# Kernel optimization log

Hardware: AMD Instinct MI355X
Metric: run time of the kernel (lower is better)

The kernel has to match this reference:

```python
import jax, jax.numpy as jnp
import numpy as np

EPS = 1.1920929e-07  # torch.finfo(float32).eps, used by F.rms_norm default

def rope(x, cos, sin):
    # x: [B,T,H,D]; cos/sin: [1,T,1,D//2]
    d = x.shape[-1] // 2
    x1, x2 = x[..., :d], x[..., d:]
    return jnp.concatenate([x1 * cos + x2 * sin, -x1 * sin + x2 * cos], axis=-1)

def rmsnorm(x):
    return x * jax.lax.rsqrt(jnp.mean(x * x, axis=-1, keepdims=True) + EPS)

def setup_inputs() -> dict:
    key = jax.random.key(0)
    ks = jax.random.split(key, 9)
    B, T, E = 2, 2048, 1024
    Hkv, D = 4, 64
    return {
        "x": jax.random.normal(ks[0], (B, T, E), jnp.float32),
        "ve": jax.random.normal(ks[1], (B, T, Hkv * D), jnp.float32),
        "cos": jax.random.normal(ks[2], (1, T, 1, D // 2), jnp.float32),
        "sin": jax.random.normal(ks[3], (1, T, 1, D // 2), jnp.float32),
        "Wq": jax.random.normal(ks[4], (E, E), jnp.float32) * 0.02,
        "Wk": jax.random.normal(ks[5], (Hkv * D, E), jnp.float32) * 0.02,
        "Wv": jax.random.normal(ks[6], (Hkv * D, E), jnp.float32) * 0.02,
        "Wproj": jax.random.normal(ks[7], (E, E), jnp.float32) * 0.02,
        "Wgate": jax.random.normal(ks[8], (Hkv, 32), jnp.float32) * 0.02,
        "window_size": 1024,
    }

def reference(x, ve, cos, sin, Wq, Wk, Wv, Wproj, Wgate, window_size):
    B, T, E = x.shape
    H, Hkv, D = 16, 4, 64
    G = H // Hkv  # GQA group size
    q = (x @ Wq.T).reshape(B, T, H, D)
    k = (x @ Wk.T).reshape(B, T, Hkv, D)
    v = (x @ Wv.T).reshape(B, T, Hkv, D)
    # value-embedding gating
    gate = 2.0 * jax.nn.sigmoid(x[..., :32] @ Wgate.T)          # [B,T,Hkv]
    v = v + gate[..., None] * ve.reshape(B, T, Hkv, D)
    # RoPE then QK RMS-norm
    q = rmsnorm(rope(q, cos, sin))
    k = rmsnorm(rope(k, cos, sin))
    # to [B,H,T,D]; repeat-interleave kv heads for GQA (matches torch enable_gqa)
    q = q.transpose(0, 2, 1, 3)
    k = jnp.repeat(k.transpose(0, 2, 1, 3), G, axis=1)
    v = jnp.repeat(v.transpose(0, 2, 1, 3), G, axis=1)
    # causal + sliding-window boolean mask
    row = jnp.arange(T)[:, None]
    col = jnp.arange(T)[None, :]
    mask = (col <= row) & (col >= row - window_size)            # [T,T]
    scale = 1.0 / jnp.sqrt(jnp.float32(D))
    scores = jnp.einsum("bhqd,bhkd->bhqk", q, k) * scale
    scores = jnp.where(mask, scores, -jnp.inf)
    p = jax.nn.softmax(scores, axis=-1)
    y = jnp.einsum("bhqk,bhkd->bhqd", p, v)
    y = y.transpose(0, 2, 1, 3).reshape(B, T, E)
    return y @ Wproj.T
```

## Files before the change

### kernel.cpp

```cpp
#include <hip/hip_runtime.h>


typedef float f32x4 __attribute__((ext_vector_type(4)));
typedef short s16x8 __attribute__((ext_vector_type(8)));
typedef short s16x4 __attribute__((ext_vector_type(4)));
typedef _Float16 f16x4 __attribute__((ext_vector_type(4)));

__device__ __forceinline__ unsigned short f2bf(float f) {
  unsigned u = __float_as_uint(f);
  u += 0x7fffu + ((u >> 16) & 1u);
  return (unsigned short)(u >> 16);
}
__device__ __forceinline__ unsigned short h16(float f) {
  _Float16 h = (_Float16)f;
  return __builtin_bit_cast(unsigned short, h);
}

__device__ __forceinline__ float fexp2(float x) {
#if __has_builtin(__builtin_amdgcn_exp2f)
  return __builtin_amdgcn_exp2f(x);
#else
  return __expf(x * 0.69314718f);
#endif
}

__device__ __forceinline__ void gl2lds16(const unsigned short* g, unsigned short* l) {
  __builtin_amdgcn_global_load_lds((const __attribute__((address_space(1))) unsigned int*)g,
                                   (__attribute__((address_space(3))) unsigned int*)l, 16, 0, 0);
}

__global__ __launch_bounds__(256) void cvt_gate(
    const float* __restrict__ x, const float* __restrict__ wq, const float* __restrict__ wk,
    const float* __restrict__ wv, const float* __restrict__ wp, const float* __restrict__ wgate,
    unsigned short* __restrict__ xb, unsigned short* __restrict__ wqkv,
    unsigned short* __restrict__ wpj, float* __restrict__ gatep) {
  int blk = blockIdx.x;
  if (blk < 6656) {
    int i = blk * 256 + threadIdx.x;
    const float* s;
    unsigned short* d;
    if (i < 1048576) { s = x; d = xb; }
    else if (i < 1310720) { i -= 1048576; s = wq; d = wqkv; }
    else if (i < 1376256) { i -= 1310720; s = wk; d = wqkv + 1048576; }
    else if (i < 1441792) { i -= 1376256; s = wv; d = wqkv + 1310720; }
    else { i -= 1441792; s = wp; d = wpj; }
    float4 v = ((const float4*)s)[i];
    ushort4 o;
    o.x = f2bf(v.x); o.y = f2bf(v.y); o.z = f2bf(v.z); o.w = f2bf(v.w);
    ((ushort4*)d)[i] = o;
  } else {
    int i = (blk - 6656) * 256 + threadIdx.x;
    int bt = i >> 2, h = i & 3;
    const float4* xp = (const float4*)(x + (size_t)bt * 1024);
    const float4* wpt = (const float4*)(wgate + h * 32);
    float s = 0.f;
#pragma unroll
    for (int j = 0; j < 8; ++j) {
      float4 a = xp[j], b = wpt[j];
      s += a.x * b.x + a.y * b.y + a.z * b.z + a.w * b.w;
    }
    gatep[i] = 2.f / (1.f + __expf(-s));
  }
}

__global__ __launch_bounds__(256) void gemm_qkv(
    const unsigned short* __restrict__ A, const unsigned short* __restrict__ B,
    const float* __restrict__ cosp, const float* __restrict__ sinp,
    const float* __restrict__ gatep, const float* __restrict__ ve,
    unsigned short* __restrict__ q_r, unsigned short* __restrict__ k_r,
    unsigned short* __restrict__ vp2) {
  __shared__ unsigned short smem[24576];
  unsigned short* As = smem;
  unsigned short* Bs = smem + 8192;
  const int K = 1024;
  int bn = blockIdx.x, bm = blockIdx.y;
  int t = threadIdx.x;
  int w = t >> 6, lane = t & 63;
  int c = lane & 15, g = lane >> 4;
  int wm = w >> 1, wn = w & 1;

  f32x4 acc[2][4];
#pragma unroll
  for (int i = 0; i < 2; ++i)
#pragma unroll
    for (int j = 0; j < 4; ++j) acc[i][j] = (f32x4){0.f, 0.f, 0.f, 0.f};

  const unsigned short* Ab = A + (size_t)(bm * 64) * K;
  const unsigned short* Bb = B + (size_t)(bn * 128) * K;
  int srow = lane >> 4;
  int sgrp = lane & 15;

  for (int k0 = 0; k0 < K; k0 += 128) {
#pragma unroll
    for (int j = 0; j < 4; ++j) {
      int r0 = w * 16 + j * 4;
      int r = r0 + srow;
      gl2lds16(Ab + (size_t)r * K + k0 + (sgrp ^ (r & 7)) * 8, As + r0 * 128);
    }
#pragma unroll
    for (int j = 0; j < 8; ++j) {
      int r0 = w * 32 + j * 4;
      int r = r0 + srow;
      gl2lds16(Bb + (size_t)r * K + k0 + (sgrp ^ (r & 7)) * 8, Bs + r0 * 128);
    }
    __syncthreads();
#pragma unroll
    for (int kk = 0; kk < 4; ++kk) {
      int sw = ((kk * 4 + g) ^ (c & 7)) * 8;
      s16x8 af[2], bf[4];
#pragma unroll
      for (int mt = 0; mt < 2; ++mt)
        af[mt] = *(const s16x8*)(As + (wm * 32 + mt * 16 + c) * 128 + sw);
#pragma unroll
      for (int nt = 0; nt < 4; ++nt)
        bf[nt] = *(const s16x8*)(Bs + (wn * 64 + nt * 16 + c) * 128 + sw);
#pragma unroll
      for (int mt = 0; mt < 2; ++mt)
#pragma unroll
        for (int nt = 0; nt < 4; ++nt)
          acc[mt][nt] = __builtin_amdgcn_mfma_f32_16x16x32_bf16(af[mt], bf[nt], acc[mt][nt], 0, 0, 0);
    }
    __syncthreads();
  }

  const float QSCL = 0.125f * 1.44269504f;
  if (bn < 10) {
    unsigned short* eb = smem + w * 2176;
#pragma unroll
    for (int mt = 0; mt < 2; ++mt) {
#pragma unroll
      for (int r = 0; r < 4; ++r) {
        int lrow = mt * 16 + g * 4 + r;
        int rowg = bm * 64 + wm * 32 + lrow;
        int tt = rowg & 2047;
        float v0 = acc[mt][0][r], v1 = acc[mt][1][r], v2 = acc[mt][2][r], v3 = acc[mt][3][r];
        float cs0 = cosp[tt * 32 + c], sn0 = sinp[tt * 32 + c];
        float cs1 = cosp[tt * 32 + 16 + c], sn1 = sinp[tt * 32 + 16 + c];
        float r0 = v0 * cs0 + v2 * sn0;
        float r1 = v1 * cs1 + v3 * sn1;
        float r2 = v2 * cs0 - v0 * sn0;
        float r3 = v3 * cs1 - v1 * sn1;
        float ss = r0 * r0 + r1 * r1 + r2 * r2 + r3 * r3;
        ss += __shfl_xor(ss, 1);
        ss += __shfl_xor(ss, 2);
        ss += __shfl_xor(ss, 4);
        ss += __shfl_xor(ss, 8);
        float sc = rsqrtf(ss * (1.0f / 64.0f) + 1.1920929e-07f);
        if (bn < 8) sc *= QSCL;
        eb[lrow * 68 + c] = f2bf(r0 * sc);
        eb[lrow * 68 + 16 + c] = f2bf(r1 * sc);
        eb[lrow * 68 + 32 + c] = f2bf(r2 * sc);
        eb[lrow * 68 + 48 + c] = f2bf(r3 * sc);
      }
    }
    asm volatile("s_waitcnt lgkmcnt(0)" ::: "memory");
#pragma unroll
    for (int j = 0; j < 4; ++j) {
      int idx = lane * 4 + j;
      int lrow = idx >> 3;
      int ck = idx & 7;
      s16x8 val = *(const s16x8*)(eb + lrow * 68 + ck * 8);
      int rowg = bm * 64 + wm * 32 + lrow;
      int b = rowg >> 11, tt = rowg & 2047;
      unsigned short* dst;
      if (bn < 8) dst = q_r + ((size_t)(b * 16 + bn * 2 + wn) * 2048 + tt) * 64 + ck * 8;
      else dst = k_r + ((size_t)(b * 4 + (bn - 8) * 2 + wn) * 2048 + tt) * 64 + ck * 8;
      *(s16x8*)dst = val;
    }
  } else {
    unsigned short* eb = smem + w * 2560;
    int h = (bn - 10) * 2 + wn;
#pragma unroll
    for (int mt = 0; mt < 2; ++mt) {
#pragma unroll
      for (int r = 0; r < 4; ++r) {
        int key = mt * 16 + g * 4 + r;
        int rowg = bm * 64 + wm * 32 + key;
        float gate = gatep[rowg * 4 + h];
        const float* vep = ve + (size_t)rowg * 256 + h * 64;
        eb[(0 * 16 + c) * 40 + key] = h16(acc[mt][0][r] + gate * vep[c]);
        eb[(1 * 16 + c) * 40 + key] = h16(acc[mt][1][r] + gate * vep[16 + c]);
        eb[(2 * 16 + c) * 40 + key] = h16(acc[mt][2][r] + gate * vep[32 + c]);
        eb[(3 * 16 + c) * 40 + key] = h16(acc[mt][3][r] + gate * vep[48 + c]);
      }
    }
    asm volatile("s_waitcnt lgkmcnt(0)" ::: "memory");
    int rowg0 = bm * 64 + wm * 32;
    int b = rowg0 >> 11;
    int tile = (rowg0 & 2047) >> 5;
    unsigned short* vb = vp2 + ((size_t)(b * 4 + h) * 64 + tile) * 2048;
#pragma unroll
    for (int j = 0; j < 4; ++j) {
      int cid = j * 64 + lane;
      int d = cid >> 2;
      int kg = cid & 3;
      s16x8 val = *(const s16x8*)(eb + d * 40 + kg * 8);
      *(s16x8*)(vb + d * 32 + kg * 8) = val;
    }
  }
}

__global__ __launch_bounds__(256) void gemm_bf16_64(
    const unsigned short* __restrict__ A, const unsigned short* __restrict__ B,
    float* __restrict__ C, int K, int ldc) {
  __shared__ unsigned short As[64 * 128];
  __shared__ unsigned short Bs[128 * 128];
  int bn = blockIdx.x, bm = blockIdx.y;
  int t = threadIdx.x;
  int w = t >> 6, lane = t & 63;
  int c = lane & 15, g = lane >> 4;
  int wm = w >> 1, wn = w & 1;

  f32x4 acc[2][4];
#pragma unroll
  for (int i = 0; i < 2; ++i)
#pragma unroll
    for (int j = 0; j < 4; ++j) acc[i][j] = (f32x4){0.f, 0.f, 0.f, 0.f};

  const unsigned short* Ab = A + (size_t)(bm * 64) * K;
  const unsigned short* Bb = B + (size_t)(bn * 128) * K;
  int srow = lane >> 4;
  int sgrp = lane & 15;

  for (int k0 = 0; k0 < K; k0 += 128) {
#pragma unroll
    for (int j = 0; j < 4; ++j) {
      int r0 = w * 16 + j * 4;
      int r = r0 + srow;
      gl2lds16(Ab + (size_t)r * K + k0 + (sgrp ^ (r & 7)) * 8, As + r0 * 128);
    }
#pragma unroll
    for (int j = 0; j < 8; ++j) {
      int r0 = w * 32 + j * 4;
      int r = r0 + srow;
      gl2lds16(Bb + (size_t)r * K + k0 + (sgrp ^ (r & 7)) * 8, Bs + r0 * 128);
    }
    __syncthreads();
#pragma unroll
    for (int kk = 0; kk < 4; ++kk) {
      int sw = ((kk * 4 + g) ^ (c & 7)) * 8;
      s16x8 af[2], bf[4];
#pragma unroll
      for (int mt = 0; mt < 2; ++mt)
        af[mt] = *(const s16x8*)(As + (wm * 32 + mt * 16 + c) * 128 + sw);
#pragma unroll
      for (int nt = 0; nt < 4; ++nt)
        bf[nt] = *(const s16x8*)(Bs + (wn * 64 + nt * 16 + c) * 128 + sw);
#pragma unroll
      for (int mt = 0; mt < 2; ++mt)
#pragma unroll
        for (int nt = 0; nt < 4; ++nt)
          acc[mt][nt] = __builtin_amdgcn_mfma_f32_16x16x32_bf16(af[mt], bf[nt], acc[mt][nt], 0, 0, 0);
    }
    __syncthreads();
  }
#pragma unroll
  for (int mt = 0; mt < 2; ++mt)
#pragma unroll
    for (int nt = 0; nt < 4; ++nt)
#pragma unroll
      for (int r = 0; r < 4; ++r) {
        int rowg = bm * 64 + wm * 32 + mt * 16 + g * 4 + r;
        int colg = bn * 128 + wn * 64 + nt * 16 + c;
        C[(size_t)rowg * ldc + colg] = acc[mt][nt][r];
      }
}

__global__ __launch_bounds__(256) void attn_kernel(
    const unsigned short* __restrict__ q_r, const unsigned short* __restrict__ k_r,
    const unsigned short* __restrict__ v_p2, unsigned short* __restrict__ y_b,
    const int* __restrict__ wptr) {
  const int W = *wptr;
  const int bid = blockIdx.x;
  const int rr = bid >> 8, cc = bid & 255;
  const int mm = cc & 7;
  const int h = (cc >> 3) & 15, b = cc >> 7;
  const int qt = (rr == 0) ? mm : (rr == 1) ? 15 - mm : (rr == 2) ? 16 + mm : 31 - mm;
  const int tid = threadIdx.x;
  const int w = tid >> 6, lane = tid & 63, c = lane & 15, g = lane >> 4;
  const int r0b = qt * 64;
  const int r0w = r0b + w * 16;
  const int hkv = h >> 2;
  const float M = 11.5415603f;

  __shared__ unsigned short Ks[2][32 * 68];
  __shared__ unsigned short Vs[2][64 * 40];

  const unsigned short* kbase = k_r + (size_t)(b * 4 + hkv) * 131072;
  const unsigned short* vbase = v_p2 + (size_t)(b * 4 + hkv) * 131072;
  const unsigned short* qbase = q_r + ((size_t)(b * 16 + h) * 2048 + r0w) * 64;

  s16x8 q_lo = *(const s16x8*)(qbase + c * 64 + g * 8);
  s16x8 q_hi = *(const s16x8*)(qbase + c * 64 + 32 + g * 8);

  int kt0w = r0w - W; if (kt0w < 0) kt0w = 0;
  const int ktEw = r0w + 16;
  int KT0 = r0b - W; if (KT0 < 0) KT0 = 0;
  KT0 &= ~31;
  const int KTE = r0b + 64;

  float l_part = 0.f;
  f32x4 acc[4];
#pragma unroll
  for (int dt = 0; dt < 4; ++dt) acc[dt] = (f32x4){0.f, 0.f, 0.f, 0.f};

  s16x8 pk = *(const s16x8*)(kbase + (size_t)KT0 * 64 + tid * 8);
  s16x8 pv = *(const s16x8*)(vbase + (size_t)(KT0 >> 5) * 2048 + tid * 8);

  const int koff = (tid >> 3) * 68 + (tid & 7) * 8;
  const int voff = (tid >> 2) * 40 + (tid & 3) * 8;

  int bufI = 0;
  for (int kt = KT0; kt < KTE; kt += 32, bufI ^= 1) {
    int nkt = (kt + 32 < KTE) ? kt + 32 : kt;
    s16x8 nk = *(const s16x8*)(kbase + (size_t)nkt * 64 + tid * 8);
    s16x8 nv = *(const s16x8*)(vbase + (size_t)(nkt >> 5) * 2048 + tid * 8);

    unsigned short* kdst = &Ks[bufI][koff];
    *(s16x4*)kdst = __builtin_shufflevector(pk, pk, 0, 1, 2, 3);
    *(s16x4*)(kdst + 4) = __builtin_shufflevector(pk, pk, 4, 5, 6, 7);
    *(s16x8*)(&Vs[bufI][voff]) = pv;
    __syncthreads();

    if (kt + 32 > kt0w && kt < ktEw) {
      const unsigned short* kr0 = &Ks[bufI][c * 68 + g * 8];
      s16x4 a0 = *(const s16x4*)(kr0);
      s16x4 a1 = *(const s16x4*)(kr0 + 4);
      s16x4 a2 = *(const s16x4*)(kr0 + 32);
      s16x4 a3 = *(const s16x4*)(kr0 + 36);
      const unsigned short* kr1 = kr0 + 16 * 68;
      s16x4 a4 = *(const s16x4*)(kr1);
      s16x4 a5 = *(const s16x4*)(kr1 + 4);
      s16x4 a6 = *(const s16x4*)(kr1 + 32);
      s16x4 a7 = *(const s16x4*)(kr1 + 36);
      s16x8 k0lo = __builtin_shufflevector(a0, a1, 0, 1, 2, 3, 4, 5, 6, 7);
      s16x8 k0hi = __builtin_shufflevector(a2, a3, 0, 1, 2, 3, 4, 5, 6, 7);
      s16x8 k1lo = __builtin_shufflevector(a4, a5, 0, 1, 2, 3, 4, 5, 6, 7);
      s16x8 k1hi = __builtin_shufflevector(a6, a7, 0, 1, 2, 3, 4, 5, 6, 7);

      f32x4 S0 = (f32x4){0.f, 0.f, 0.f, 0.f};
      f32x4 S1 = (f32x4){0.f, 0.f, 0.f, 0.f};
      S0 = __builtin_amdgcn_mfma_f32_16x16x32_bf16(k0lo, q_lo, S0, 0, 0, 0);
      S0 = __builtin_amdgcn_mfma_f32_16x16x32_bf16(k0hi, q_hi, S0, 0, 0, 0);
      S1 = __builtin_amdgcn_mfma_f32_16x16x32_bf16(k1lo, q_lo, S1, 0, 0, 0);
      S1 = __builtin_amdgcn_mfma_f32_16x16x32_bf16(k1hi, q_hi, S1, 0, 0, 0);

      f16x4 P0, P1;
      const bool edge = (kt < kt0w + 32) || (kt + 32 > r0w);
      const int qrow = r0w + c;
#pragma unroll
      for (int r = 0; r < 4; ++r) {
        float p0 = fexp2(S0[r] - M);
        float p1 = fexp2(S1[r] - M);
        if (edge) {
          int k0i = kt + g * 4 + r;
          int k1i = k0i + 16;
          if (!(k0i <= qrow && k0i >= qrow - W)) p0 = 0.f;
          if (!(k1i <= qrow && k1i >= qrow - W)) p1 = 0.f;
        }
        l_part += p0 + p1;
        P0[r] = (_Float16)p0;
        P1[r] = (_Float16)p1;
      }

#pragma unroll
      for (int dt = 0; dt < 4; ++dt) {
        const unsigned short* vr = &Vs[bufI][(dt * 16 + c) * 40 + g * 4];
        f16x4 va = *(const f16x4*)(vr);
        f16x4 vb = *(const f16x4*)(vr + 16);
        acc[dt] = __builtin_amdgcn_mfma_f32_16x16x16f16(va, P0, acc[dt], 0, 0, 0);
        acc[dt] = __builtin_amdgcn_mfma_f32_16x16x16f16(vb, P1, acc[dt], 0, 0, 0);
      }
    }
    pk = nk; pv = nv;
  }

  float l = l_part;
  l += __shfl_xor(l, 16);
  l += __shfl_xor(l, 32);
  float inv = 1.0f / l;

  unsigned short* ob = y_b + ((size_t)(b * 2048 + r0w + c) * 16 + h) * 64 + g * 4;
#pragma unroll
  for (int dt = 0; dt < 4; ++dt) {
    ushort4 o;
    o.x = f2bf(acc[dt][0] * inv);
    o.y = f2bf(acc[dt][1] * inv);
    o.z = f2bf(acc[dt][2] * inv);
    o.w = f2bf(acc[dt][3] * inv);
    *(ushort4*)(ob + dt * 16) = o;
  }
}

extern "C" void kernel_launch(void* const* d_in, const int* in_sizes, int n_in,
                              void* d_out, int out_size, void* d_ws, size_t ws_size,
                              hipStream_t stream) {
  const float* x = (const float*)d_in[0];
  const float* ve = (const float*)d_in[1];
  const float* cosp = (const float*)d_in[2];
  const float* sinp = (const float*)d_in[3];
  const float* Wq = (const float*)d_in[4];
  const float* Wk = (const float*)d_in[5];
  const float* Wv = (const float*)d_in[6];
  const float* Wproj = (const float*)d_in[7];
  const float* Wgate = (const float*)d_in[8];
  const int* wptr = (const int*)d_in[9];

  unsigned short* xb = (unsigned short*)d_ws;
  unsigned short* wqkv = xb + 4194304;
  unsigned short* wpj = wqkv + 1572864;
  unsigned short* q_r = wpj + 1048576;
  unsigned short* k_r = q_r + 4194304;
  unsigned short* y_b = k_r + 1048576;
  unsigned short* vp2 = y_b + 4194304;
  float* gatep = (float*)(vp2 + 1048576);

  cvt_gate<<<6720, 256, 0, stream>>>(x, Wq, Wk, Wv, Wproj, Wgate, xb, wqkv, wpj, gatep);
  gemm_qkv<<<dim3(12, 64), 256, 0, stream>>>(xb, wqkv, cosp, sinp, gatep, ve, q_r, k_r, vp2);
  attn_kernel<<<1024, 256, 0, stream>>>(q_r, k_r, vp2, y_b, wptr);
  gemm_bf16_64<<<dim3(8, 64), 256, 0, stream>>>(y_b, wpj, (float*)d_out, 1024, 1024);
}
```

Before: 166.5 us.

## Load K/V tiles directly from global memory per wave instead of shared staging

The attention kernel no longer stages K and V tiles through double-buffered shared memory with block-wide barriers. Each wave now reads its K and V fragments straight from global memory (relying on L1/L2) and iterates only over its own key range, which removes the __syncthreads and the loop iterations spent on tiles outside that wave's window. The cost is redundant global/cache traffic, since the four waves in a block no longer share the loaded tiles, and there is no explicit prefetch to hide load latency.

```diff
diff --git a/kernel.cpp b/kernel.cpp
--- a/kernel.cpp
+++ b/kernel.cpp
@@ -278,13 +278,9 @@
   const int qt = (rr == 0) ? mm : (rr == 1) ? 15 - mm : (rr == 2) ? 16 + mm : 31 - mm;
   const int tid = threadIdx.x;
   const int w = tid >> 6, lane = tid & 63, c = lane & 15, g = lane >> 4;
-  const int r0b = qt * 64;
-  const int r0w = r0b + w * 16;
+  const int r0w = qt * 64 + w * 16;
   const int hkv = h >> 2;
   const float M = 11.5415603f;
-
-  __shared__ unsigned short Ks[2][32 * 68];
-  __shared__ unsigned short Vs[2][64 * 40];
 
   const unsigned short* kbase = k_r + (size_t)(b * 4 + hkv) * 131072;
   const unsigned short* vbase = v_p2 + (size_t)(b * 4 + hkv) * 131072;
@@ -294,85 +290,56 @@
   s16x8 q_hi = *(const s16x8*)(qbase + c * 64 + 32 + g * 8);
 
   int kt0w = r0w - W; if (kt0w < 0) kt0w = 0;
-  const int ktEw = r0w + 16;
-  int KT0 = r0b - W; if (KT0 < 0) KT0 = 0;
-  KT0 &= ~31;
-  const int KTE = r0b + 64;
+  const int KT0 = kt0w & ~31;
+  const int KTE = r0w + 16;
 
   float l_part = 0.f;
   f32x4 acc[4];
 #pragma unroll
   for (int dt = 0; dt < 4; ++dt) acc[dt] = (f32x4){0.f, 0.f, 0.f, 0.f};
 
-  s16x8 pk = *(const s16x8*)(kbase + (size_t)KT0 * 64 + tid * 8);
-  s16x8 pv = *(const s16x8*)(vbase + (size_t)(KT0 >> 5) * 2048 + tid * 8);
-
-  const int koff = (tid >> 3) * 68 + (tid & 7) * 8;
-  const int voff = (tid >> 2) * 40 + (tid & 3) * 8;
-
-  int bufI = 0;
-  for (int kt = KT0; kt < KTE; kt += 32, bufI ^= 1) {
-    int nkt = (kt + 32 < KTE) ? kt + 32 : kt;
-    s16x8 nk = *(const s16x8*)(kbase + (size_t)nkt * 64 + tid * 8);
-    s16x8 nv = *(const s16x8*)(vbase + (size_t)(nkt >> 5) * 2048 + tid * 8);
-
-    unsigned short* kdst = &Ks[bufI][koff];
-    *(s16x4*)kdst = __builtin_shufflevector(pk, pk, 0, 1, 2, 3);
-    *(s16x4*)(kdst + 4) = __builtin_shufflevector(pk, pk, 4, 5, 6, 7);
-    *(s16x8*)(&Vs[bufI][voff]) = pv;
-    __syncthreads();
-
-    if (kt + 32 > kt0w && kt < ktEw) {
-      const unsigned short* kr0 = &Ks[bufI][c * 68 + g * 8];
-      s16x4 a0 = *(const s16x4*)(kr0);
-      s16x4 a1 = *(const s16x4*)(kr0 + 4);
-      s16x4 a2 = *(const s16x4*)(kr0 + 32);
-      s16x4 a3 = *(const s16x4*)(kr0 + 36);
-      const unsigned short* kr1 = kr0 + 16 * 68;
-      s16x4 a4 = *(const s16x4*)(kr1);
-      s16x4 a5 = *(const s16x4*)(kr1 + 4);
-      s16x4 a6 = *(const s16x4*)(kr1 + 32);
-      s16x4 a7 = *(const s16x4*)(kr1 + 36);
-      s16x8 k0lo = __builtin_shufflevector(a0, a1, 0, 1, 2, 3, 4, 5, 6, 7);
-      s16x8 k0hi = __builtin_shufflevector(a2, a3, 0, 1, 2, 3, 4, 5, 6, 7);
-      s16x8 k1lo = __builtin_shufflevector(a4, a5, 0, 1, 2, 3, 4, 5, 6, 7);
-      s16x8 k1hi = __builtin_shufflevector(a6, a7, 0, 1, 2, 3, 4, 5, 6, 7);
-
-      f32x4 S0 = (f32x4){0.f, 0.f, 0.f, 0.f};
-      f32x4 S1 = (f32x4){0.f, 0.f, 0.f, 0.f};
-      S0 = __builtin_amdgcn_mfma_f32_16x16x32_bf16(k0lo, q_lo, S0, 0, 0, 0);
-      S0 = __builtin_amdgcn_mfma_f32_16x16x32_bf16(k0hi, q_hi, S0, 0, 0, 0);
-      S1 = __builtin_amdgcn_mfma_f32_16x16x32_bf16(k1lo, q_lo, S1, 0, 0, 0);
-      S1 = __builtin_amdgcn_mfma_f32_16x16x32_bf16(k1hi, q_hi, S1, 0, 0, 0);
-
-      f16x4 P0, P1;
-      const bool edge = (kt < kt0w + 32) || (kt + 32 > r0w);
-      const int qrow = r0w + c;
-#pragma unroll
-      for (int r = 0; r < 4; ++r) {
-        float p0 = fexp2(S0[r] - M);
-        float p1 = fexp2(S1[r] - M);
-        if (edge) {
-          int k0i = kt + g * 4 + r;
-          int k1i = k0i + 16;
-          if (!(k0i <= qrow && k0i >= qrow - W)) p0 = 0.f;
-          if (!(k1i <= qrow && k1i >= qrow - W)) p1 = 0.f;
-        }
-        l_part += p0 + p1;
-        P0[r] = (_Float16)p0;
-        P1[r] = (_Float16)p1;
+  const int qrow = r0w + c;
+
+  for (int kt = KT0; kt < KTE; kt += 32) {
+    const unsigned short* kr = kbase + (size_t)(kt + c) * 64 + g * 8;
+    s16x8 k0lo = *(const s16x8*)(kr);
+    s16x8 k0hi = *(const s16x8*)(kr + 32);
+    s16x8 k1lo = *(const s16x8*)(kr + 16 * 64);
+    s16x8 k1hi = *(const s16x8*)(kr + 16 * 64 + 32);
+
+    f32x4 S0 = (f32x4){0.f, 0.f, 0.f, 0.f};
+    f32x4 S1 = (f32x4){0.f, 0.f, 0.f, 0.f};
+    S0 = __builtin_amdgcn_mfma_f32_16x16x32_bf16(k0lo, q_lo, S0, 0, 0, 0);
+    S0 = __builtin_amdgcn_mfma_f32_16x16x32_bf16(k0hi, q_hi, S0, 0, 0, 0);
+    S1 = __builtin_amdgcn_mfma_f32_16x16x32_bf16(k1lo, q_lo, S1, 0, 0, 0);
+    S1 = __builtin_amdgcn_mfma_f32_16x16x32_bf16(k1hi, q_hi, S1, 0, 0, 0);
+
+    f16x4 P0, P1;
+    const bool edge = (kt < kt0w + 32) || (kt + 32 > r0w);
+#pragma unroll
+    for (int r = 0; r < 4; ++r) {
+      float p0 = fexp2(S0[r] - M);
+      float p1 = fexp2(S1[r] - M);
+      if (edge) {
+        int k0i = kt + g * 4 + r;
+        int k1i = k0i + 16;
+        if (!(k0i <= qrow && k0i >= qrow - W)) p0 = 0.f;
+        if (!(k1i <= qrow && k1i >= qrow - W)) p1 = 0.f;
       }
-
-#pragma unroll
-      for (int dt = 0; dt < 4; ++dt) {
-        const unsigned short* vr = &Vs[bufI][(dt * 16 + c) * 40 + g * 4];
-        f16x4 va = *(const f16x4*)(vr);
-        f16x4 vb = *(const f16x4*)(vr + 16);
-        acc[dt] = __builtin_amdgcn_mfma_f32_16x16x16f16(va, P0, acc[dt], 0, 0, 0);
-        acc[dt] = __builtin_amdgcn_mfma_f32_16x16x16f16(vb, P1, acc[dt], 0, 0, 0);
-      }
-    }
-    pk = nk; pv = nv;
+      l_part += p0 + p1;
+      P0[r] = (_Float16)p0;
+      P1[r] = (_Float16)p1;
+    }
+
+    const unsigned short* vt = vbase + (size_t)(kt >> 5) * 2048;
+#pragma unroll
+    for (int dt = 0; dt < 4; ++dt) {
+      const unsigned short* vr = vt + (dt * 16 + c) * 32 + g * 4;
+      f16x4 va = *(const f16x4*)(vr);
+      f16x4 vb = *(const f16x4*)(vr + 16);
+      acc[dt] = __builtin_amdgcn_mfma_f32_16x16x16f16(va, P0, acc[dt], 0, 0, 0);
+      acc[dt] = __builtin_amdgcn_mfma_f32_16x16x16f16(vb, P1, acc[dt], 0, 0, 0);
+    }
   }
 
   float l = l_part;
```

Result: slower. 222.0 us (+33.3%).

## Double-buffer output projection GEMM with larger 128x128 tiles

Applied to the files above, without the earlier changes.

Replaces the 64x128-tile projection GEMM with a 128x128-tile version that double-buffers its A/B tiles in LDS. The next K-slice is prefetched while the current one is computed, and one of the two barriers per iteration is removed. The goal is to hide global-load latency and improve operand reuse. The trade-off is more LDS and registers per block, fewer blocks in the grid, and a K loop count fixed at 8.

```diff
diff --git a/kernel.cpp b/kernel.cpp
--- a/kernel.cpp
+++ b/kernel.cpp
@@ -200,67 +200,70 @@
   }
 }
 
-__global__ __launch_bounds__(256) void gemm_bf16_64(
+__global__ __launch_bounds__(256) void gemm_bf16_128(
     const unsigned short* __restrict__ A, const unsigned short* __restrict__ B,
     float* __restrict__ C, int K, int ldc) {
-  __shared__ unsigned short As[64 * 128];
-  __shared__ unsigned short Bs[128 * 128];
+  __shared__ unsigned short As[2][128 * 128];
+  __shared__ unsigned short Bs[2][128 * 128];
   int bn = blockIdx.x, bm = blockIdx.y;
   int t = threadIdx.x;
   int w = t >> 6, lane = t & 63;
   int c = lane & 15, g = lane >> 4;
   int wm = w >> 1, wn = w & 1;
 
-  f32x4 acc[2][4];
-#pragma unroll
-  for (int i = 0; i < 2; ++i)
+  f32x4 acc[4][4];
+#pragma unroll
+  for (int i = 0; i < 4; ++i)
 #pragma unroll
     for (int j = 0; j < 4; ++j) acc[i][j] = (f32x4){0.f, 0.f, 0.f, 0.f};
 
-  const unsigned short* Ab = A + (size_t)(bm * 64) * K;
+  const unsigned short* Ab = A + (size_t)(bm * 128) * K;
   const unsigned short* Bb = B + (size_t)(bn * 128) * K;
   int srow = lane >> 4;
   int sgrp = lane & 15;
 
-  for (int k0 = 0; k0 < K; k0 += 128) {
-#pragma unroll
-    for (int j = 0; j < 4; ++j) {
-      int r0 = w * 16 + j * 4;
-      int r = r0 + srow;
-      gl2lds16(Ab + (size_t)r * K + k0 + (sgrp ^ (r & 7)) * 8, As + r0 * 128);
-    }
-#pragma unroll
-    for (int j = 0; j < 8; ++j) {
-      int r0 = w * 32 + j * 4;
-      int r = r0 + srow;
-      gl2lds16(Bb + (size_t)r * K + k0 + (sgrp ^ (r & 7)) * 8, Bs + r0 * 128);
-    }
+#define STAGE128(buf, k0)                                                          \
+  {                                                                                \
+    _Pragma("unroll")                                                              \
+    for (int j = 0; j < 8; ++j) {                                                  \
+      int r0 = w * 32 + j * 4;                                                     \
+      int r = r0 + srow;                                                           \
+      gl2lds16(Ab + (size_t)r * K + (k0) + (sgrp ^ (r & 7)) * 8, &As[buf][r0 * 128]); \
+      gl2lds16(Bb + (size_t)r * K + (k0) + (sgrp ^ (r & 7)) * 8, &Bs[buf][r0 * 128]); \
+    }                                                                              \
+  }
+
+  STAGE128(0, 0);
+  for (int tstep = 0; tstep < 8; ++tstep) {
+    int buf = tstep & 1;
     __syncthreads();
+    if (tstep < 7) STAGE128(buf ^ 1, (tstep + 1) * 128);
 #pragma unroll
     for (int kk = 0; kk < 4; ++kk) {
       int sw = ((kk * 4 + g) ^ (c & 7)) * 8;
-      s16x8 af[2], bf[4];
-#pragma unroll
-      for (int mt = 0; mt < 2; ++mt)
-        af[mt] = *(const s16x8*)(As + (wm * 32 + mt * 16 + c) * 128 + sw);
+      s16x8 af[4], bf[4];
+#pragma unroll
+      for (int mt = 0; mt < 4; ++mt)
+        af[mt] = *(const s16x8*)(&As[buf][(wm * 64 + mt * 16 + c) * 128 + sw]);
 #pragma unroll
       for (int nt = 0; nt < 4; ++nt)
-        bf[nt] = *(const s16x8*)(Bs + (wn * 64 + nt * 16 + c) * 128 + sw);
-#pragma unroll
-      for (int mt = 0; mt < 2; ++mt)
+        bf[nt] = *(const s16x8*)(&Bs[buf][(wn * 64 + nt * 16 + c) * 128 + sw]);
+#pragma unroll
+      for (int mt = 0; mt < 4; ++mt)
 #pragma unroll
         for (int nt = 0; nt < 4; ++nt)
           acc[mt][nt] = __builtin_amdgcn_mfma_f32_16x16x32_bf16(af[mt], bf[nt], acc[mt][nt], 0, 0, 0);
     }
-    __syncthreads();
-  }
-#pragma unroll
-  for (int mt = 0; mt < 2; ++mt)
+  }
+#undef STAGE128
+
+#pragma unroll
+  for (int mt = 0; mt < 4; ++mt)
 #pragma unroll
     for (int nt = 0; nt < 4; ++nt)
 #pragma unroll
       for (int r = 0; r < 4; ++r) {
-        int rowg = bm * 64 + wm * 32 + mt * 16 + g * 4 + r;
+        int rowg = bm * 128 + wm * 64 + mt * 16 + g * 4 + r;
         int colg = bn * 128 + wn * 64 + nt * 16 + c;
         C[(size_t)rowg * ldc + colg] = acc[mt][nt][r];
       }
@@ -418,5 +421,5 @@
   cvt_gate<<<6720, 256, 0, stream>>>(x, Wq, Wk, Wv, Wproj, Wgate, xb, wqkv, wpj, gatep);
   gemm_qkv<<<dim3(12, 64), 256, 0, stream>>>(xb, wqkv, cosp, sinp, gatep, ve, q_r, k_r, vp2);
   attn_kernel<<<1024, 256, 0, stream>>>(q_r, k_r, vp2, y_b, wptr);
-  gemm_bf16_64<<<dim3(8, 64), 256, 0, stream>>>(y_b, wpj, (float*)d_out, 1024, 1024);
-}
+  gemm_bf16_128<<<dim3(8, 32), 256, 0, stream>>>(y_b, wpj, (float*)d_out, 1024, 1024);
+}
```

After: 168.0 us. Within noise of the previous version (+0.9%).
